# Performance work log

Measured on AMD Instinct MI355X. Metric: run time of the kernel, lower is better.

## Reference

```python
import jax, jax.numpy as jnp
import numpy as np


def setup_inputs() -> dict:
    key = jax.random.key(0)
    k1, _ = jax.random.split(key)
    x = jax.random.normal(k1, (2, 16, 16, 16, 64), dtype=jnp.float32)
    gamma = jnp.ones((1,), dtype=jnp.float32)  # learned scalar (zeros at init; ones to make output nontrivial)
    return {"x": x, "gamma": gamma}


def reference(x, gamma):
    # x: (B, D, H, W, C); faithful to the Keras layer: flatten spatial dims,
    # energy = Q @ Q^T over the N=D*H*W axis, softmax(axis=-1), attn @ Q,
    # then gamma-scaled residual add.
    B, D, H, W, C = x.shape
    N = D * H * W
    q = x.reshape(B, N, C)                            # proj_query (B, N, C)
    energy = jnp.einsum('bnc,bmc->bnm', q, q)          # (B, N, N)
    attn = jax.nn.softmax(energy, axis=-1)
    out = jnp.einsum('bnm,bmc->bnc', attn, q)          # (B, N, C)
    out = out.reshape(B, D, H, W, C)
    return gamma * out + x
```

## Files before the change

### kernel.cpp

```cpp
#include <hip/hip_runtime.h>
#include <hip/hip_bf16.h>
#include <math.h>


#define NN 4096
#define CC 64
#define LOG2E 1.4426950408889634f

typedef __attribute__((ext_vector_type(4))) float f32x4;
typedef __attribute__((ext_vector_type(8))) short bf16x8;
typedef __attribute__((ext_vector_type(4))) short bf16x4;
typedef unsigned short u16;
typedef __attribute__((ext_vector_type(4))) u16 u16x4;
typedef __attribute__((ext_vector_type(2))) unsigned u32x2;

__device__ inline u16 f2bf(float f) {
  union { float f; unsigned u; } v; v.f = f;
  unsigned r = (v.u + 0x7fffu + ((v.u >> 16) & 1u)) >> 16;
  return (u16)r;
}
__device__ inline float bf2f(short h) {
  union { unsigned u; float f; } v;
  v.u = ((unsigned)(unsigned short)h) << 16;
  return v.f;
}
__device__ inline unsigned fbits(float f) {
  union { float f; unsigned u; } v; v.f = f;
  return v.u;
}
__device__ inline bf16x8 cvt8(f32x4 a, f32x4 b) {
  bf16x8 r;
  r[0] = (short)f2bf(a[0]); r[1] = (short)f2bf(a[1]);
  r[2] = (short)f2bf(a[2]); r[3] = (short)f2bf(a[3]);
  r[4] = (short)f2bf(b[0]); r[5] = (short)f2bf(b[1]);
  r[6] = (short)f2bf(b[2]); r[7] = (short)f2bf(b[3]);
  return r;
}

__global__ __launch_bounds__(256) void prep_kernel(const float* __restrict__ x,
                                                   u16* __restrict__ Qb,
                                                   u16* __restrict__ Vt) {
  __shared__ u16 t[64][20];
  int b = blockIdx.x >> 8;
  int n0 = (blockIdx.x & 255) << 4;
  const f32x4* x4 = (const f32x4*)(x + ((size_t)b * NN + n0) * CC);
  u16* qb = Qb + ((size_t)b * NN + n0) * CC;
  {
    int idx4 = threadIdx.x;
    int i = idx4 >> 4, cg = idx4 & 15;
    f32x4 v = x4[idx4];
    u16x4 h;
    h[0] = f2bf(v[0]); h[1] = f2bf(v[1]); h[2] = f2bf(v[2]); h[3] = f2bf(v[3]);
    *(u16x4*)(qb + (size_t)i * CC + cg * 4) = h;
    t[cg * 4 + 0][i] = h[0]; t[cg * 4 + 1][i] = h[1];
    t[cg * 4 + 2][i] = h[2]; t[cg * 4 + 3][i] = h[3];
  }
  __syncthreads();
  int kb = n0 >> 6, kw0 = n0 & 63;
  {
    int idx4 = threadIdx.x;
    int c = idx4 >> 2, i4 = (idx4 & 3) * 4;
    u16x4 h = *(const u16x4*)(&t[c][i4]);
    *(u16x4*)(Vt + (((size_t)b * (NN / 64) + kb) * 64 + c) * 64 + kw0 + i4) = h;
  }
}

template <int S>
__global__ __launch_bounds__(256, 4) void attn_split(
    const u16* __restrict__ Qb, const u16* __restrict__ Vt,
    u16* __restrict__ Opart, float* __restrict__ lpart) {
  constexpr int KPS = NN / S;
  constexpr int ITERS = KPS / 64;
  const int w = threadIdx.x >> 6;
  const int lane = threadIdx.x & 63;
  const int quad = lane >> 4, col = lane & 15;
  const int blk = blockIdx.x;
  const int b = blk / (64 * S);
  const int rg = (blk / S) & 63;
  const int s = blk % S;

  __shared__ u16 KT[2][64 * 64];
  __shared__ u16 VT[2][64 * 64];
  __shared__ u16 PB[4][16 * 64];

  const u16* Qbase = Qb + (size_t)b * NN * CC;
  const u16* Vbase = Vt + (size_t)b * NN * CC;
  const int row0 = rg * 64 + w * 16;

  bf16x8 qs0, qs1;
  float m_sc;
  {
    const u16* qp = Qbase + (size_t)(row0 + col) * CC + quad * 8;
    bf16x8 r0 = *(const bf16x8*)qp;
    bf16x8 r1 = *(const bf16x8*)(qp + 32);
    float msum = 0.f;
#pragma unroll
    for (int j = 0; j < 8; ++j) {
      float a0 = bf2f(r0[j]), a1 = bf2f(r1[j]);
      u16 h0 = f2bf(a0 * LOG2E), h1 = f2bf(a1 * LOG2E);
      qs0[j] = (short)h0; qs1[j] = (short)h1;
      msum += bf2f((short)h0) * a0 + bf2f((short)h1) * a1;
    }
    msum += __shfl_xor(msum, 16);
    msum += __shfl_xor(msum, 32);
    m_sc = msum;
  }

  f32x4 zero = {0.f, 0.f, 0.f, 0.f};
  f32x4 acc[4] = {zero, zero, zero, zero};
  float l_loc = 0.f;

  const int kk = lane >> 3;
  const int sw = (lane & 7) ^ kk;
  const u16* kptr = Qbase + (size_t)(s * KPS + w * 16 + kk) * CC + sw * 8;
  const u16* vptr = Vbase + ((size_t)(s * KPS >> 6) * 64 + (w * 16 + kk)) * 64 + sw * 8;

#define STAGE(p, kp, vp)                                                      \
  {                                                                           \
    _Pragma("unroll")                                                         \
    for (int g = 0; g < 2; ++g) {                                             \
      __builtin_amdgcn_global_load_lds(                                       \
          (const __attribute__((address_space(1))) unsigned*)((kp) + g * 512),\
          (__attribute__((address_space(3))) unsigned*)&KT[p][(w * 16 + g * 8) * 64], \
          16, 0, 0);                                                          \
      __builtin_amdgcn_global_load_lds(                                       \
          (const __attribute__((address_space(1))) unsigned*)((vp) + g * 512),\
          (__attribute__((address_space(3))) unsigned*)&VT[p][(w * 16 + g * 8) * 64], \
          16, 0, 0);                                                          \
    }                                                                         \
  }

  STAGE(0, kptr, vptr)
  const int cs = col & 7;
  u16* PBw = &PB[w][0];
#pragma unroll 2
  for (int i = 0; i < ITERS; ++i) {
    __syncthreads();
    const int p = i & 1;
    if (i + 1 < ITERS) STAGE(p ^ 1, kptr + 4096, vptr + 4096)
    kptr += 4096; vptr += 4096;

    f32x4 sx[4];
#pragma unroll
    for (int t = 0; t < 4; ++t) {
      bf16x8 ka = *(const bf16x8*)&KT[p][(t * 16 + col) * 64 + (quad ^ cs) * 8];
      bf16x8 kb = *(const bf16x8*)&KT[p][(t * 16 + col) * 64 + ((quad + 4) ^ cs) * 8];
      sx[t] = __builtin_amdgcn_mfma_f32_16x16x32_bf16(ka, qs0, zero, 0, 0, 0);
      sx[t] = __builtin_amdgcn_mfma_f32_16x16x32_bf16(kb, qs1, sx[t], 0, 0, 0);
    }
#pragma unroll
    for (int t = 0; t < 4; ++t) {
      f32x4 pv;
#pragma unroll
      for (int r = 0; r < 4; ++r) pv[r] = exp2f(sx[t][r] - m_sc);
      l_loc += pv[0] + pv[1] + pv[2] + pv[3];
      u32x2 d;
      d[0] = __builtin_amdgcn_perm(fbits(pv[1]), fbits(pv[0]), 0x07060302u);
      d[1] = __builtin_amdgcn_perm(fbits(pv[3]), fbits(pv[2]), 0x07060302u);
      *(u32x2*)&PBw[col * 64 + ((t * 2 + (quad >> 1)) ^ cs) * 8 + (quad & 1) * 4] = d;
    }
    bf16x8 pf0 = *(const bf16x8*)&PBw[col * 64 + (quad ^ cs) * 8];
    bf16x8 pf1 = *(const bf16x8*)&PBw[col * 64 + ((quad + 4) ^ cs) * 8];
#pragma unroll
    for (int cg = 0; cg < 4; ++cg) {
      bf16x8 va = *(const bf16x8*)&VT[p][(cg * 16 + col) * 64 + (quad ^ cs) * 8];
      bf16x8 vb = *(const bf16x8*)&VT[p][(cg * 16 + col) * 64 + ((quad + 4) ^ cs) * 8];
      acc[cg] = __builtin_amdgcn_mfma_f32_16x16x32_bf16(pf0, va, acc[cg], 0, 0, 0);
      acc[cg] = __builtin_amdgcn_mfma_f32_16x16x32_bf16(pf1, vb, acc[cg], 0, 0, 0);
    }
  }
#undef STAGE

  size_t pbase = (((size_t)(b * 64 + rg)) * S + s) * (64 * 64);
  size_t lbase = (((size_t)(b * 64 + rg)) * S + s) * 64;
  {
    float l = l_loc;
    l += __shfl_xor(l, 16);
    l += __shfl_xor(l, 32);
    if (quad == 0) lpart[lbase + w * 16 + col] = l;
  }
#pragma unroll
  for (int r = 0; r < 4; ++r) {
    int lr = w * 16 + quad * 4 + r;
    size_t o = pbase + (size_t)lr * 64;
    Opart[o + col]      = f2bf(acc[0][r]);
    Opart[o + col + 16] = f2bf(acc[1][r]);
    Opart[o + col + 32] = f2bf(acc[2][r]);
    Opart[o + col + 48] = f2bf(acc[3][r]);
  }
}

template <int S>
__global__ __launch_bounds__(256) void epi_kernel(
    const float* __restrict__ x, const float* __restrict__ gamma,
    const u16* __restrict__ Opart, const float* __restrict__ lpart,
    float* __restrict__ out) {
  int t = blockIdx.x * 256 + threadIdx.x;
  int cg = t & 15;
  int n = (t >> 4) & (NN - 1);
  int b = t >> 16;
  int rb = n >> 6, lr = n & 63;
  size_t obase = ((size_t)(b * 64 + rb) * S) * 4096 + (size_t)lr * 64 + cg * 4;
  size_t lbase = ((size_t)(b * 64 + rb) * S) * 64 + lr;
  f32x4 sO = {0.f, 0.f, 0.f, 0.f};
  float sL = 0.f;
#pragma unroll
  for (int s = 0; s < S; ++s) {
    u16x4 o4 = *(const u16x4*)(Opart + obase + (size_t)s * 4096);
    sL += lpart[lbase + s * 64];
    sO[0] += bf2f((short)o4[0]); sO[1] += bf2f((short)o4[1]);
    sO[2] += bf2f((short)o4[2]); sO[3] += bf2f((short)o4[3]);
  }
  size_t xi = (((size_t)b * NN + n) * CC + cg * 4);
  f32x4 xv = *(const f32x4*)(x + xi);
  float g = gamma[0], inv = 1.f / sL;
  f32x4 ov;
#pragma unroll
  for (int j = 0; j < 4; ++j) ov[j] = g * (sO[j] * inv) + xv[j];
  *(f32x4*)(((float*)out) + xi) = ov;
}

template <int WPB>
__global__ __launch_bounds__(WPB * 64, 4) void attn_fast(
    const float* __restrict__ x, const float* __restrict__ gamma,
    const u16* __restrict__ Qb, const u16* __restrict__ Vt,
    float* __restrict__ out) {
  const int w = threadIdx.x >> 6;
  const int lane = threadIdx.x & 63;
  const int quad = lane >> 4, col = lane & 15;
  const int b = blockIdx.x >> 8;
  const int tile = (blockIdx.x & 255) << 4;

  extern __shared__ char smem[];
  float* Osh = (float*)smem;
  float* lsh = Osh + WPB * 1024;
  u16* pl = (u16*)(lsh + WPB * 16) + w * 2176;

  const size_t xoff = (size_t)b * NN * CC;
  const u16* Qbase = Qb + xoff;
  const u16* Vbase = Vt + xoff;

  bf16x8 qf0 = *(const bf16x8*)(Qbase + (size_t)(tile + col) * CC + quad * 8);
  bf16x8 qf1 = *(const bf16x8*)(Qbase + (size_t)(tile + col) * CC + 32 + quad * 8);

  float msum = 0.f;
#pragma unroll
  for (int j = 0; j < 8; ++j) {
    float a = bf2f(qf0[j]), c = bf2f(qf1[j]);
    msum += a * a + c * c;
  }
  msum += __shfl_xor(msum, 16);
  msum += __shfl_xor(msum, 32);
  float m_i[4];
#pragma unroll
  for (int r = 0; r < 4; ++r) m_i[r] = __shfl(msum, quad * 4 + r);

  f32x4 zero = {0.f, 0.f, 0.f, 0.f};
  f32x4 acc[4] = {zero, zero, zero, zero};
  float l_i[4] = {0.f, 0.f, 0.f, 0.f};

  const int k0 = w * (NN / WPB);
#pragma unroll 2
  for (int kt = k0; kt < k0 + NN / WPB; kt += 64) {
    u16* plc = pl + ((kt >> 6) & 1) * 1088;
    f32x4 sx[4];
#pragma unroll
    for (int t = 0; t < 4; ++t) {
      const u16* kp = Qbase + (size_t)(kt + t * 16 + col) * CC + quad * 8;
      bf16x8 ka = *(const bf16x8*)kp;
      bf16x8 kb = *(const bf16x8*)(kp + 32);
      sx[t] = __builtin_amdgcn_mfma_f32_16x16x32_bf16(qf0, ka, zero, 0, 0, 0);
      sx[t] = __builtin_amdgcn_mfma_f32_16x16x32_bf16(qf1, kb, sx[t], 0, 0, 0);
    }
#pragma unroll
    for (int t = 0; t < 4; ++t) {
#pragma unroll
      for (int r = 0; r < 4; ++r) {
        float p = __expf(sx[t][r] - m_i[r]);
        l_i[r] += p;
        plc[(quad * 4 + r) * 68 + t * 16 + col] = f2bf(p);
      }
    }
    bf16x8 pf0 = *(const bf16x8*)(plc + col * 68 + quad * 8);
    bf16x8 pf1 = *(const bf16x8*)(plc + col * 68 + 32 + quad * 8);
#pragma unroll
    for (int cg = 0; cg < 4; ++cg) {
      const u16* vp = Vbase + (((size_t)(kt >> 6)) * 64 + cg * 16 + col) * 64 + quad * 8;
      bf16x8 v0 = *(const bf16x8*)vp;
      bf16x8 v1 = *(const bf16x8*)(vp + 32);
      acc[cg] = __builtin_amdgcn_mfma_f32_16x16x32_bf16(pf0, v0, acc[cg], 0, 0, 0);
      acc[cg] = __builtin_amdgcn_mfma_f32_16x16x32_bf16(pf1, v1, acc[cg], 0, 0, 0);
    }
  }

#pragma unroll
  for (int r = 0; r < 4; ++r)
#pragma unroll
    for (int off = 1; off < 16; off <<= 1) l_i[r] += __shfl_xor(l_i[r], off, 16);
#pragma unroll
  for (int r = 0; r < 4; ++r) {
    int row = quad * 4 + r;
    Osh[(w * 16 + row) * 64 + col]      = acc[0][r];
    Osh[(w * 16 + row) * 64 + col + 16] = acc[1][r];
    Osh[(w * 16 + row) * 64 + col + 32] = acc[2][r];
    Osh[(w * 16 + row) * 64 + col + 48] = acc[3][r];
    if (col == 0) lsh[w * 16 + row] = l_i[r];
  }
  __syncthreads();

  float g = gamma[0];
  for (int row = w; row < 16; row += WPB) {
    float L = 0.f, val = 0.f;
#pragma unroll
    for (int w2 = 0; w2 < WPB; ++w2) {
      L += lsh[w2 * 16 + row];
      val += Osh[(w2 * 16 + row) * 64 + lane];
    }
    size_t o = xoff + (size_t)(tile + row) * CC + lane;
    out[o] = g * (val / L) + x[o];
  }
}

template <int WPB>
__global__ __launch_bounds__(512) void attn_fb(const float* __restrict__ x,
                                               const float* __restrict__ gamma,
                                               float* __restrict__ out) {
  const int w = threadIdx.x >> 6;
  const int lane = threadIdx.x & 63;
  const int quad = lane >> 4, col = lane & 15;
  const int b = blockIdx.x >> 8;
  const int tile = (blockIdx.x & 255) << 4;

  extern __shared__ char smem[];
  float* Osh = (float*)smem;
  float* msh = Osh + WPB * 1024;
  float* lsh = msh + WPB * 16;
  u16* pl = (u16*)(lsh + WPB * 16) + w * 768;
  u16* vt = (u16*)(lsh + WPB * 16) + WPB * 768 + w * 2176;

  const size_t xoff = (size_t)b * NN * CC;
  const f32x4* x4 = (const f32x4*)(x + xoff);

  bf16x8 qf0, qf1;
  {
    int ri = (tile + col) * 16 + quad * 2;
    qf0 = cvt8(x4[ri], x4[ri + 1]);
    qf1 = cvt8(x4[ri + 8], x4[ri + 9]);
  }
  f32x4 zero = {0.f, 0.f, 0.f, 0.f};
  f32x4 acc0 = zero, acc1 = zero, acc2 = zero, acc3 = zero;
  float m_i[4], l_i[4];
#pragma unroll
  for (int r = 0; r < 4; ++r) { m_i[r] = -1e30f; l_i[r] = 0.f; }

  const int k0 = w * (NN / WPB);
  for (int kt = k0; kt < k0 + NN / WPB; kt += 32) {
    bf16x8 k00, k01, k10, k11;
    {
      int kb = (kt + col) * 16 + quad * 2;
      k00 = cvt8(x4[kb], x4[kb + 1]);
      k01 = cvt8(x4[kb + 8], x4[kb + 9]);
      k10 = cvt8(x4[kb + 256], x4[kb + 257]);
      k11 = cvt8(x4[kb + 264], x4[kb + 265]);
#pragma unroll
      for (int h = 0; h < 2; ++h) {
        bf16x8 va = h ? k10 : k00, vb = h ? k11 : k01;
        int base = (h * 16 + col) * 68 + quad * 8;
        *(bf16x4*)(vt + base) = __builtin_shufflevector(va, va, 0, 1, 2, 3);
        *(bf16x4*)(vt + base + 4) = __builtin_shufflevector(va, va, 4, 5, 6, 7);
        *(bf16x4*)(vt + base + 32) = __builtin_shufflevector(vb, vb, 0, 1, 2, 3);
        *(bf16x4*)(vt + base + 36) = __builtin_shufflevector(vb, vb, 4, 5, 6, 7);
      }
    }
    f32x4 s0 = zero, s1 = zero;
    s0 = __builtin_amdgcn_mfma_f32_16x16x32_bf16(qf0, k00, s0, 0, 0, 0);
    s0 = __builtin_amdgcn_mfma_f32_16x16x32_bf16(qf1, k01, s0, 0, 0, 0);
    s1 = __builtin_amdgcn_mfma_f32_16x16x32_bf16(qf0, k10, s1, 0, 0, 0);
    s1 = __builtin_amdgcn_mfma_f32_16x16x32_bf16(qf1, k11, s1, 0, 0, 0);

    float p0[4], p1[4], alpha[4];
#pragma unroll
    for (int r = 0; r < 4; ++r) {
      float mx = fmaxf(s0[r], s1[r]);
#pragma unroll
      for (int off = 1; off < 16; off <<= 1) mx = fmaxf(mx, __shfl_xor(mx, off, 16));
      float mn = fmaxf(m_i[r], mx);
      alpha[r] = __expf(m_i[r] - mn);
      p0[r] = __expf(s0[r] - mn);
      p1[r] = __expf(s1[r] - mn);
      float rs = p0[r] + p1[r];
#pragma unroll
      for (int off = 1; off < 16; off <<= 1) rs += __shfl_xor(rs, off, 16);
      l_i[r] = l_i[r] * alpha[r] + rs;
      m_i[r] = mn;
    }
#pragma unroll
    for (int r = 0; r < 4; ++r) {
      acc0[r] *= alpha[r]; acc1[r] *= alpha[r];
      acc2[r] *= alpha[r]; acc3[r] *= alpha[r];
    }
#pragma unroll
    for (int r = 0; r < 4; ++r) {
      pl[(quad * 4 + r) * 24 + col] = f2bf(p0[r]);
      pl[384 + (quad * 4 + r) * 24 + col] = f2bf(p1[r]);
    }
    bf16x8 pf = *(const bf16x8*)(pl + (quad >> 1) * 384 + col * 24 + (quad & 1) * 8);

    bf16x8 v0, v1, v2, v3;
#pragma unroll
    for (int j = 0; j < 8; ++j) {
      int rb = (quad * 8 + j) * 68 + col;
      v0[j] = (short)vt[rb];
      v1[j] = (short)vt[rb + 16];
      v2[j] = (short)vt[rb + 32];
      v3[j] = (short)vt[rb + 48];
    }
    acc0 = __builtin_amdgcn_mfma_f32_16x16x32_bf16(pf, v0, acc0, 0, 0, 0);
    acc1 = __builtin_amdgcn_mfma_f32_16x16x32_bf16(pf, v1, acc1, 0, 0, 0);
    acc2 = __builtin_amdgcn_mfma_f32_16x16x32_bf16(pf, v2, acc2, 0, 0, 0);
    acc3 = __builtin_amdgcn_mfma_f32_16x16x32_bf16(pf, v3, acc3, 0, 0, 0);
  }

#pragma unroll
  for (int r = 0; r < 4; ++r) {
    int row = quad * 4 + r;
    Osh[(w * 16 + row) * 64 + col] = acc0[r];
    Osh[(w * 16 + row) * 64 + col + 16] = acc1[r];
    Osh[(w * 16 + row) * 64 + col + 32] = acc2[r];
    Osh[(w * 16 + row) * 64 + col + 48] = acc3[r];
    if (col == 0) { msh[w * 16 + row] = m_i[r]; lsh[w * 16 + row] = l_i[r]; }
  }
  __syncthreads();

  float g = gamma[0];
  for (int row = w; row < 16; row += WPB) {
    float M = -1e30f;
#pragma unroll
    for (int w2 = 0; w2 < WPB; ++w2) M = fmaxf(M, msh[w2 * 16 + row]);
    float L = 0.f, val = 0.f;
#pragma unroll
    for (int w2 = 0; w2 < WPB; ++w2) {
      float e = __expf(msh[w2 * 16 + row] - M);
      L += lsh[w2 * 16 + row] * e;
      val += Osh[(w2 * 16 + row) * 64 + lane] * e;
    }
    size_t o = xoff + (size_t)(tile + row) * CC + lane;
    out[o] = g * (val / L) + x[o];
  }
}

extern "C" void kernel_launch(void* const* d_in, const int* in_sizes, int n_in,
                              void* d_out, int out_size, void* d_ws, size_t ws_size,
                              hipStream_t stream) {
  const float* x = (const float*)d_in[0];
  const float* gamma = (const float*)d_in[1];
  float* out = (float*)d_out;

  constexpr int S = 8;
  constexpr size_t kQV = (size_t)2 * 2 * NN * CC * sizeof(u16);
  constexpr size_t kOp = (size_t)2 * 64 * S * 64 * 64 * sizeof(u16);
  constexpr size_t kLp = (size_t)2 * 64 * S * 64 * sizeof(float);
  if (ws_size >= kQV + kOp + kLp) {
    u16* Qb = (u16*)d_ws;
    u16* Vt = Qb + (size_t)2 * NN * CC;
    u16* Opart = (u16*)((char*)d_ws + kQV);
    float* lpart = (float*)((char*)d_ws + kQV + kOp);
    prep_kernel<<<512, 256, 0, stream>>>(x, Qb, Vt);
    attn_split<S><<<2 * 64 * S, 256, 0, stream>>>(Qb, Vt, Opart, lpart);
    epi_kernel<S><<<(2 * NN * 16) / 256, 256, 0, stream>>>(x, gamma, Opart, lpart, out);
  } else if (ws_size >= kQV) {
    u16* Qb = (u16*)d_ws;
    u16* Vt = Qb + (size_t)2 * NN * CC;
    prep_kernel<<<512, 256, 0, stream>>>(x, Qb, Vt);
    constexpr int SM = 8 * 1024 * 4 + 8 * 16 * 4 + 8 * 2176 * 2;
    attn_fast<8><<<512, 512, SM, stream>>>(x, gamma, Qb, Vt, out);
  } else {
    constexpr int SM4 = 4 * (1024 + 32) * 4 + 4 * 768 * 2 + 4 * 2176 * 2;
    attn_fb<4><<<512, 256, SM4, stream>>>(x, gamma, out);
  }
}
```

Before: 82.16 us.

## Load K/V directly from global, fold max into MFMA init, sum rows via MFMA

Drops the double-buffered LDS staging of K and V tiles and the per-iteration __syncthreads. Each wave now reads its K and V fragments straight from global memory, relying on L1/L2 to serve the four waves that read the same tile. The score offset -m_sc is fed in as the MFMA accumulator init instead of being subtracted per element. The softmax denominator is computed by an extra MFMA against a ones vector instead of scalar adds and shuffles. This removes barrier stalls and LDS traffic, but it quadruples global/cache request traffic and exposes load latency without explicit prefetch.

```diff
diff --git a/kernel.cpp b/kernel.cpp
--- a/kernel.cpp
+++ b/kernel.cpp
@@ -79,8 +79,6 @@
   const int rg = (blk / S) & 63;
   const int s = blk % S;
 
-  __shared__ u16 KT[2][64 * 64];
-  __shared__ u16 VT[2][64 * 64];
   __shared__ u16 PB[4][16 * 64];
 
   const u16* Qbase = Qb + (size_t)b * NN * CC;
@@ -108,52 +106,32 @@
 
   f32x4 zero = {0.f, 0.f, 0.f, 0.f};
   f32x4 acc[4] = {zero, zero, zero, zero};
-  float l_loc = 0.f;
-
-  const int kk = lane >> 3;
-  const int sw = (lane & 7) ^ kk;
-  const u16* kptr = Qbase + (size_t)(s * KPS + w * 16 + kk) * CC + sw * 8;
-  const u16* vptr = Vbase + ((size_t)(s * KPS >> 6) * 64 + (w * 16 + kk)) * 64 + sw * 8;
-
-#define STAGE(p, kp, vp)                                                      \
-  {                                                                           \
-    _Pragma("unroll")                                                         \
-    for (int g = 0; g < 2; ++g) {                                             \
-      __builtin_amdgcn_global_load_lds(                                       \
-          (const __attribute__((address_space(1))) unsigned*)((kp) + g * 512),\
-          (__attribute__((address_space(3))) unsigned*)&KT[p][(w * 16 + g * 8) * 64], \
-          16, 0, 0);                                                          \
-      __builtin_amdgcn_global_load_lds(                                       \
-          (const __attribute__((address_space(1))) unsigned*)((vp) + g * 512),\
-          (__attribute__((address_space(3))) unsigned*)&VT[p][(w * 16 + g * 8) * 64], \
-          16, 0, 0);                                                          \
-    }                                                                         \
-  }
-
-  STAGE(0, kptr, vptr)
+  f32x4 accl = zero;
+  f32x4 cinit = {-m_sc, -m_sc, -m_sc, -m_sc};
+  bf16x8 onesb;
+#pragma unroll
+  for (int j = 0; j < 8; ++j) onesb[j] = (short)0x3F80;
+
   const int cs = col & 7;
   u16* PBw = &PB[w][0];
+  const u16* kl = Qbase + (size_t)(s * KPS + col) * CC + quad * 8;
+  const u16* vl = Vbase + (size_t)(s * KPS + col) * CC + quad * 8;
+
 #pragma unroll 2
   for (int i = 0; i < ITERS; ++i) {
-    __syncthreads();
-    const int p = i & 1;
-    if (i + 1 < ITERS) STAGE(p ^ 1, kptr + 4096, vptr + 4096)
-    kptr += 4096; vptr += 4096;
-
     f32x4 sx[4];
 #pragma unroll
     for (int t = 0; t < 4; ++t) {
-      bf16x8 ka = *(const bf16x8*)&KT[p][(t * 16 + col) * 64 + (quad ^ cs) * 8];
-      bf16x8 kb = *(const bf16x8*)&KT[p][(t * 16 + col) * 64 + ((quad + 4) ^ cs) * 8];
-      sx[t] = __builtin_amdgcn_mfma_f32_16x16x32_bf16(ka, qs0, zero, 0, 0, 0);
+      bf16x8 ka = *(const bf16x8*)(kl + t * 1024);
+      bf16x8 kb = *(const bf16x8*)(kl + t * 1024 + 32);
+      sx[t] = __builtin_amdgcn_mfma_f32_16x16x32_bf16(ka, qs0, cinit, 0, 0, 0);
       sx[t] = __builtin_amdgcn_mfma_f32_16x16x32_bf16(kb, qs1, sx[t], 0, 0, 0);
     }
 #pragma unroll
     for (int t = 0; t < 4; ++t) {
       f32x4 pv;
 #pragma unroll
-      for (int r = 0; r < 4; ++r) pv[r] = exp2f(sx[t][r] - m_sc);
-      l_loc += pv[0] + pv[1] + pv[2] + pv[3];
+      for (int r = 0; r < 4; ++r) pv[r] = exp2f(sx[t][r]);
       u32x2 d;
       d[0] = __builtin_amdgcn_perm(fbits(pv[1]), fbits(pv[0]), 0x07060302u);
       d[1] = __builtin_amdgcn_perm(fbits(pv[3]), fbits(pv[2]), 0x07060302u);
@@ -161,23 +139,23 @@
     }
     bf16x8 pf0 = *(const bf16x8*)&PBw[col * 64 + (quad ^ cs) * 8];
     bf16x8 pf1 = *(const bf16x8*)&PBw[col * 64 + ((quad + 4) ^ cs) * 8];
+    accl = __builtin_amdgcn_mfma_f32_16x16x32_bf16(pf0, onesb, accl, 0, 0, 0);
+    accl = __builtin_amdgcn_mfma_f32_16x16x32_bf16(pf1, onesb, accl, 0, 0, 0);
 #pragma unroll
     for (int cg = 0; cg < 4; ++cg) {
-      bf16x8 va = *(const bf16x8*)&VT[p][(cg * 16 + col) * 64 + (quad ^ cs) * 8];
-      bf16x8 vb = *(const bf16x8*)&VT[p][(cg * 16 + col) * 64 + ((quad + 4) ^ cs) * 8];
+      bf16x8 va = *(const bf16x8*)(vl + cg * 1024);
+      bf16x8 vb = *(const bf16x8*)(vl + cg * 1024 + 32);
       acc[cg] = __builtin_amdgcn_mfma_f32_16x16x32_bf16(pf0, va, acc[cg], 0, 0, 0);
       acc[cg] = __builtin_amdgcn_mfma_f32_16x16x32_bf16(pf1, vb, acc[cg], 0, 0, 0);
     }
-  }
-#undef STAGE
+    kl += 4096; vl += 4096;
+  }
 
   size_t pbase = (((size_t)(b * 64 + rg)) * S + s) * (64 * 64);
   size_t lbase = (((size_t)(b * 64 + rg)) * S + s) * 64;
-  {
-    float l = l_loc;
-    l += __shfl_xor(l, 16);
-    l += __shfl_xor(l, 32);
-    if (quad == 0) lpart[lbase + w * 16 + col] = l;
+  if (col == 0) {
+#pragma unroll
+    for (int r = 0; r < 4; ++r) lpart[lbase + w * 16 + quad * 4 + r] = accl[r];
   }
 #pragma unroll
   for (int r = 0; r < 4; ++r) {
```

Result: slower. 122.7 us (+49.3%).

## Restructure attention loop with explicit vmcnt pipelining and MFMA-based row sums

Applied to the files above, without the earlier changes.

Replaces __syncthreads with explicit s_waitcnt vmcnt plus two raw barriers per iteration. Both K/V stages are prefetched up front, and the next stage is issued into the buffer just consumed. The max subtraction is folded into the MFMA accumulator init, and the softmax denominator is computed by an extra MFMA of P against a ones vector instead of VALU adds and shuffles. s_setprio hints and full unrolling are added. The intent is to cut VALU work and overlap global loads with compute, at the cost of an extra barrier and two extra MFMAs per iteration. The row sum now uses bf16-rounded P, which matches the numerator.

```diff
diff --git a/kernel.cpp b/kernel.cpp
--- a/kernel.cpp
+++ b/kernel.cpp
@@ -108,7 +108,11 @@
 
   f32x4 zero = {0.f, 0.f, 0.f, 0.f};
   f32x4 acc[4] = {zero, zero, zero, zero};
-  float l_loc = 0.f;
+  f32x4 accl = zero;
+  f32x4 cinit = {-m_sc, -m_sc, -m_sc, -m_sc};
+  bf16x8 onesb;
+#pragma unroll
+  for (int j = 0; j < 8; ++j) onesb[j] = (short)0x3F80;
 
   const int kk = lane >> 3;
   const int sw = (lane & 7) ^ kk;
@@ -131,29 +135,36 @@
   }
 
   STAGE(0, kptr, vptr)
+  STAGE(1, kptr + 4096, vptr + 4096)
   const int cs = col & 7;
   u16* PBw = &PB[w][0];
-#pragma unroll 2
+
+#pragma unroll
   for (int i = 0; i < ITERS; ++i) {
-    __syncthreads();
+    if (i + 1 < ITERS)
+      asm volatile("s_waitcnt vmcnt(4)" ::: "memory");
+    else
+      asm volatile("s_waitcnt vmcnt(0)" ::: "memory");
+    __builtin_amdgcn_sched_barrier(0);
+    __builtin_amdgcn_s_barrier();
+    __builtin_amdgcn_sched_barrier(0);
     const int p = i & 1;
-    if (i + 1 < ITERS) STAGE(p ^ 1, kptr + 4096, vptr + 4096)
-    kptr += 4096; vptr += 4096;
 
     f32x4 sx[4];
+    __builtin_amdgcn_s_setprio(1);
 #pragma unroll
     for (int t = 0; t < 4; ++t) {
       bf16x8 ka = *(const bf16x8*)&KT[p][(t * 16 + col) * 64 + (quad ^ cs) * 8];
       bf16x8 kb = *(const bf16x8*)&KT[p][(t * 16 + col) * 64 + ((quad + 4) ^ cs) * 8];
-      sx[t] = __builtin_amdgcn_mfma_f32_16x16x32_bf16(ka, qs0, zero, 0, 0, 0);
+      sx[t] = __builtin_amdgcn_mfma_f32_16x16x32_bf16(ka, qs0, cinit, 0, 0, 0);
       sx[t] = __builtin_amdgcn_mfma_f32_16x16x32_bf16(kb, qs1, sx[t], 0, 0, 0);
     }
+    __builtin_amdgcn_s_setprio(0);
 #pragma unroll
     for (int t = 0; t < 4; ++t) {
       f32x4 pv;
 #pragma unroll
-      for (int r = 0; r < 4; ++r) pv[r] = exp2f(sx[t][r] - m_sc);
-      l_loc += pv[0] + pv[1] + pv[2] + pv[3];
+      for (int r = 0; r < 4; ++r) pv[r] = exp2f(sx[t][r]);
       u32x2 d;
       d[0] = __builtin_amdgcn_perm(fbits(pv[1]), fbits(pv[0]), 0x07060302u);
       d[1] = __builtin_amdgcn_perm(fbits(pv[3]), fbits(pv[2]), 0x07060302u);
@@ -161,6 +172,9 @@
     }
     bf16x8 pf0 = *(const bf16x8*)&PBw[col * 64 + (quad ^ cs) * 8];
     bf16x8 pf1 = *(const bf16x8*)&PBw[col * 64 + ((quad + 4) ^ cs) * 8];
+    __builtin_amdgcn_s_setprio(1);
+    accl = __builtin_amdgcn_mfma_f32_16x16x32_bf16(pf0, onesb, accl, 0, 0, 0);
+    accl = __builtin_amdgcn_mfma_f32_16x16x32_bf16(pf1, onesb, accl, 0, 0, 0);
 #pragma unroll
     for (int cg = 0; cg < 4; ++cg) {
       bf16x8 va = *(const bf16x8*)&VT[p][(cg * 16 + col) * 64 + (quad ^ cs) * 8];
@@ -168,16 +182,20 @@
       acc[cg] = __builtin_amdgcn_mfma_f32_16x16x32_bf16(pf0, va, acc[cg], 0, 0, 0);
       acc[cg] = __builtin_amdgcn_mfma_f32_16x16x32_bf16(pf1, vb, acc[cg], 0, 0, 0);
     }
+    __builtin_amdgcn_s_setprio(0);
+    __builtin_amdgcn_sched_barrier(0);
+    __builtin_amdgcn_s_barrier();
+    __builtin_amdgcn_sched_barrier(0);
+    if (i + 2 < ITERS) STAGE(p, kptr + 8192, vptr + 8192)
+    kptr += 4096; vptr += 4096;
   }
 #undef STAGE
 
   size_t pbase = (((size_t)(b * 64 + rg)) * S + s) * (64 * 64);
   size_t lbase = (((size_t)(b * 64 + rg)) * S + s) * 64;
-  {
-    float l = l_loc;
-    l += __shfl_xor(l, 16);
-    l += __shfl_xor(l, 32);
-    if (quad == 0) lpart[lbase + w * 16 + col] = l;
+  if (col == 0) {
+#pragma unroll
+    for (int r = 0; r < 4; ++r) lpart[lbase + w * 16 + quad * 4 + r] = accl[r];
   }
 #pragma unroll
   for (int r = 0; r < 4; ++r) {
```

Measured after the change: 81.36 us. No clear change (-1.0%).
